# Kernel optimization log

Hardware: AMD Instinct MI355X
Metric: run time of the kernel (lower is better)

## Reference

```python
import jax, jax.numpy as jnp
import numpy as np

EPS = 1e-8
NEG = -1e9


def setup_inputs() -> dict:
    key = jax.random.key(0)
    k = jax.random.split(key, 5)
    B, C, T, D = 32, 512, 2000, 128
    return {
        "x": jax.random.normal(k[0], (B, C, T), dtype=jnp.float32),
        "attn_w": jax.random.normal(k[1], (D, 3 * C), dtype=jnp.float32) * 0.02,
        "attn_b": jax.random.normal(k[2], (D,), dtype=jnp.float32) * 0.02,
        "ctx_w": jax.random.normal(k[3], (C, D), dtype=jnp.float32) * 0.02,
        "ctx_b": jax.random.normal(k[4], (C,), dtype=jnp.float32) * 0.02,
        "mask": jnp.ones((B, T), dtype=jnp.int32),
    }


def reference(x, attn_w, attn_b, ctx_w, ctx_b, mask):
    # x: (B, C, T); mask: (B, T) with 1 = valid frame
    m = mask.astype(x.dtype)[:, None, :]                      # (B, 1, T)
    lengths = jnp.sum(m, axis=2, keepdims=True)               # (B, 1, 1)
    mean = jnp.sum(x * m, axis=2, keepdims=True) / lengths    # (B, C, 1)
    var = jnp.sum(jnp.square(x - mean) * m, axis=2, keepdims=True) / lengths
    std = jnp.sqrt(jnp.clip(var, EPS))                        # (B, C, 1)
    # global context: concat [x, mean, std] along channels -> (B, 3C, T)
    T = x.shape[2]
    context = jnp.concatenate(
        [x, jnp.broadcast_to(mean, x.shape), jnp.broadcast_to(std, x.shape)], axis=1
    )
    # two 1x1 convs == channel GEMMs
    alpha = jnp.tanh(jnp.einsum("dc,bct->bdt", attn_w, context) + attn_b[None, :, None])
    alpha = jnp.einsum("cd,bdt->bct", ctx_w, alpha) + ctx_b[None, :, None]  # (B, C, T)
    alpha = jnp.where(m == 0, NEG, alpha)
    alpha = jax.nn.softmax(alpha, axis=2)
    pooled_mean = jnp.sum(alpha * x, axis=2)                  # (B, C)
    pooled_var = jnp.sum(alpha * jnp.square(x - pooled_mean[:, :, None]), axis=2)
    pooled_std = jnp.sqrt(jnp.clip(pooled_var, EPS))
    return jnp.concatenate([pooled_mean, pooled_std], axis=1)  # (B, 2C)
```

## Files before the change

kernel.cpp:

```cpp
#include <hip/hip_runtime.h>
#include <hip/hip_bf16.h>
#include <math.h>

#define EPSF 1e-8f
typedef __attribute__((ext_vector_type(8))) short short8;
typedef __attribute__((ext_vector_type(4))) float f32x4;

__device__ __forceinline__ float wred_sum(float v) {
#pragma unroll
  for (int o = 32; o > 0; o >>= 1) v += __shfl_down(v, o, 64);
  return v;
}

static __device__ __forceinline__ unsigned short f2bf(float f) {
  __hip_bfloat16 h = __float2bfloat16(f);
  return *reinterpret_cast<unsigned short*>(&h);
}
static __device__ __forceinline__ float bf2f(unsigned short u) {
  unsigned int v = ((unsigned int)u) << 16;
  float f;
  __builtin_memcpy(&f, &v, 4);
  return f;
}

__global__ __launch_bounds__(256) void k_zc(
    const float* __restrict__ attn_w, const float* __restrict__ ctx_w,
    unsigned short* __restrict__ awb, unsigned short* __restrict__ cwb,
    float* __restrict__ zp, int nz4, int C, int D) {
  int i = blockIdx.x * 256 + threadIdx.x;
  int DC = D * C;
  if (i < DC) {
    int d = i / C, c = i % C;
    awb[i] = f2bf(attn_w[(size_t)d * 3 * C + c]);
  } else if (i < 2 * DC) {
    int j = i - DC;
    cwb[j] = f2bf(ctx_w[j]);
  }
  if (i < nz4)
    *reinterpret_cast<float4*>(zp + (size_t)i * 4) = (float4){0.f, 0.f, 0.f, 0.f};
}

__global__ __launch_bounds__(256) void k_ms_tr(
    const float* __restrict__ x, const int* __restrict__ mask,
    float* __restrict__ sums, unsigned short* __restrict__ xbT, int C, int T) {
  int b = blockIdx.z, c0 = blockIdx.x * 64, t0 = blockIdx.y * 64;
  int tid = threadIdx.x;
  int row = tid >> 2, q = tid & 3;
  __shared__ float Xs[64][65];
  const float* xr = x + ((size_t)b * C + c0 + row) * T;
  const int* mr = mask + (size_t)b * T;
  float s1 = 0.f, s2 = 0.f;

#pragma unroll
  for (int ss = 0; ss < 4; ss++) {
    int cc = q + 4 * ss;
    int t = t0 + cc * 4;
    float4 v;
    float mv[4];
    if (t + 3 < T) {
      v = *reinterpret_cast<const float4*>(&xr[t]);
      int4 mm = *reinterpret_cast<const int4*>(&mr[t]);
      mv[0] = (float)mm.x; mv[1] = (float)mm.y; mv[2] = (float)mm.z; mv[3] = (float)mm.w;
    } else {
      v.x = (t < T) ? xr[t] : 0.f;     mv[0] = (t < T) ? (float)mr[t] : 0.f;
      v.y = (t+1 < T) ? xr[t+1] : 0.f; mv[1] = (t+1 < T) ? (float)mr[t+1] : 0.f;
      v.z = (t+2 < T) ? xr[t+2] : 0.f; mv[2] = (t+2 < T) ? (float)mr[t+2] : 0.f;
      v.w = (t+3 < T) ? xr[t+3] : 0.f; mv[3] = (t+3 < T) ? (float)mr[t+3] : 0.f;
    }
    s1 += mv[0]*v.x + mv[1]*v.y + mv[2]*v.z + mv[3]*v.w;
    s2 += mv[0]*v.x*v.x + mv[1]*v.y*v.y + mv[2]*v.z*v.z + mv[3]*v.w*v.w;
    int tl = cc * 4;
    Xs[row][tl+0] = v.x; Xs[row][tl+1] = v.y; Xs[row][tl+2] = v.z; Xs[row][tl+3] = v.w;
  }
  __syncthreads();
  {
    int trow = tid >> 2;
    int t = t0 + trow;
    if (t < T) {
      unsigned short buf[16];
#pragma unroll
      for (int m = 0; m < 16; m++) buf[m] = f2bf(Xs[q * 16 + m][trow]);
      unsigned short* dst = &xbT[((size_t)b * T + t) * C + c0 + q * 16];
      *reinterpret_cast<short8*>(dst) = *reinterpret_cast<short8*>(&buf[0]);
      *reinterpret_cast<short8*>(dst + 8) = *reinterpret_cast<short8*>(&buf[8]);
    }
  }
  s1 += __shfl_down(s1, 2, 4); s1 += __shfl_down(s1, 1, 4);
  s2 += __shfl_down(s2, 2, 4); s2 += __shfl_down(s2, 1, 4);
  if (q == 0) {
    float* sp = &sums[((size_t)b * C + c0 + row) * 2];
    atomicAdd(sp, s1);
    atomicAdd(sp + 1, s2);
  }
}

__global__ __launch_bounds__(256) void k_bias2f(
    const float* __restrict__ attn_w, const float* __restrict__ attn_b,
    const float* __restrict__ sums, const int* __restrict__ mask,
    float* __restrict__ bias2, int C, int D, int T) {
  int bd = blockIdx.x;
  int b = bd / D;
  int d = bd % D;
  int tid = threadIdx.x;
  const int* mr = mask + (size_t)b * T;
  float sl = 0.f;
  for (int t = tid; t < T; t += 256) sl += (float)mr[t];
  __shared__ float rl[4];
  sl = wred_sum(sl);
  if ((tid & 63) == 0) rl[tid >> 6] = sl;
  __syncthreads();
  float L = fmaxf(rl[0] + rl[1] + rl[2] + rl[3], 1.f);

  const float* wr = attn_w + (size_t)d * 3 * C;
  float s = 0.f;
  for (int c = tid; c < C; c += 256) {
    float s1 = sums[((size_t)b * C + c) * 2];
    float s2 = sums[((size_t)b * C + c) * 2 + 1];
    float mu = s1 / L;
    float var = s2 / L - mu * mu;
    float sd = sqrtf(fmaxf(var, EPSF));
    s += wr[C + c] * mu + wr[2 * C + c] * sd;
  }
  __shared__ float r[4];
  s = wred_sum(s);
  if ((tid & 63) == 0) r[tid >> 6] = s;
  __syncthreads();
  if (tid == 0) bias2[bd] = attn_b[d] + r[0] + r[1] + r[2] + r[3];
}

__global__ __launch_bounds__(256) void k_gemm1(
    const unsigned short* __restrict__ xbT, const unsigned short* __restrict__ awb,
    const float* __restrict__ bias2, unsigned short* __restrict__ alphaT,
    int C, int T, int D) {
  int b = blockIdx.y;
  int t0 = blockIdx.x * 64;
  int tid = threadIdx.x;
  int w = tid >> 6, lane = tid & 63;
  int l15 = lane & 15, g = lane >> 4;
  __shared__ unsigned short As[64][72];
  __shared__ unsigned short Bs[128][72];
  f32x4 acc[4][2];
#pragma unroll
  for (int i = 0; i < 4; i++)
#pragma unroll
    for (int j = 0; j < 2; j++) acc[i][j] = (f32x4){0.f, 0.f, 0.f, 0.f};

  int ar = tid >> 2, aq = tid & 3;
  int dr = tid >> 1, h = tid & 1;
  bool okA = (t0 + ar) < T;
  size_t rowA = ((size_t)b * T + t0 + ar) * C + aq * 16;
  size_t rowB = (size_t)dr * C + h * 32;

  short8 ra[2], rb[4];
  ra[0] = okA ? *reinterpret_cast<const short8*>(&xbT[rowA]) : (short8){};
  ra[1] = okA ? *reinterpret_cast<const short8*>(&xbT[rowA + 8]) : (short8){};
#pragma unroll
  for (int qq = 0; qq < 4; qq++)
    rb[qq] = *reinterpret_cast<const short8*>(&awb[rowB + qq * 8]);

  for (int c0 = 0; c0 < C; c0 += 64) {
    __syncthreads();
    *reinterpret_cast<short8*>(&As[ar][aq * 16]) = ra[0];
    *reinterpret_cast<short8*>(&As[ar][aq * 16 + 8]) = ra[1];
#pragma unroll
    for (int qq = 0; qq < 4; qq++)
      *reinterpret_cast<short8*>(&Bs[dr][h * 32 + qq * 8]) = rb[qq];
    if (c0 + 64 < C) {
      size_t nA = rowA + c0 + 64, nB = rowB + c0 + 64;
      ra[0] = okA ? *reinterpret_cast<const short8*>(&xbT[nA]) : (short8){};
      ra[1] = okA ? *reinterpret_cast<const short8*>(&xbT[nA + 8]) : (short8){};
#pragma unroll
      for (int qq = 0; qq < 4; qq++)
        rb[qq] = *reinterpret_cast<const short8*>(&awb[nB + qq * 8]);
    }
    __syncthreads();
#pragma unroll
    for (int ks = 0; ks < 2; ks++) {
      short8 a[4], bb[2];
#pragma unroll
      for (int tf = 0; tf < 4; tf++)
        a[tf] = *reinterpret_cast<const short8*>(&As[tf * 16 + l15][ks * 32 + g * 8]);
#pragma unroll
      for (int df = 0; df < 2; df++)
        bb[df] = *reinterpret_cast<const short8*>(&Bs[w * 32 + df * 16 + l15][ks * 32 + g * 8]);
#pragma unroll
      for (int tf = 0; tf < 4; tf++)
#pragma unroll
        for (int df = 0; df < 2; df++)
          acc[tf][df] = __builtin_amdgcn_mfma_f32_16x16x32_bf16(a[tf], bb[df], acc[tf][df], 0, 0, 0);
    }
  }
#pragma unroll
  for (int df = 0; df < 2; df++) {
    int d = w * 32 + df * 16 + l15;
    float bias = bias2[(size_t)b * D + d];
#pragma unroll
    for (int tf = 0; tf < 4; tf++)
#pragma unroll
      for (int r = 0; r < 4; r++) {
        int t = t0 + tf * 16 + g * 4 + r;
        if (t < T)
          alphaT[((size_t)b * T + t) * D + d] = f2bf(tanhf(bias + acc[tf][df][r]));
      }
  }
}

__global__ __launch_bounds__(256) void k_pool2(
    const unsigned short* __restrict__ alphaT, const unsigned short* __restrict__ cwb,
    const unsigned short* __restrict__ xbT, const int* __restrict__ mask,
    float* __restrict__ Sacc, int C, int T, int D) {
  int b = blockIdx.z;
  int c0 = blockIdx.y * 64;
  int ch0 = blockIdx.x * 256;
  int tid = threadIdx.x;
  int w = tid >> 6, lane = tid & 63, l15 = lane & 15, g = lane >> 4;
  __shared__ unsigned short Bl[2][64][136];
  __shared__ unsigned short Xt[2][64][72];

  short8 a[4];
#pragma unroll
  for (int ks = 0; ks < 4; ks++)
    a[ks] = *reinterpret_cast<const short8*>(
        &cwb[(size_t)(c0 + w * 16 + l15) * D + ks * 32 + g * 8]);
  int cbase = c0 + w * 16 + g * 4;
  float S0[4] = {0.f, 0.f, 0.f, 0.f};
  float S1[4] = {0.f, 0.f, 0.f, 0.f};
  float S2[4] = {0.f, 0.f, 0.f, 0.f};

  const int* mr = mask + (size_t)b * T;
  int srow = tid >> 2, sq = tid & 3;

  int rem = T - ch0;
  int ntt = rem >= 256 ? 4 : (rem + 63) >> 6;

  short8 pa0, pa1, pa2, pa3, px0, px1;

#define LOADSUB(st)                                                            \
  {                                                                            \
    int trow = ch0 + (st) * 64 + srow;                                         \
    pa0 = pa1 = pa2 = pa3 = px0 = px1 = (short8){};                            \
    if (trow < T) {                                                            \
      const unsigned short* sa = &alphaT[((size_t)b * T + trow) * D + sq * 32];\
      pa0 = *reinterpret_cast<const short8*>(sa);                              \
      pa1 = *reinterpret_cast<const short8*>(sa + 8);                          \
      pa2 = *reinterpret_cast<const short8*>(sa + 16);                         \
      pa3 = *reinterpret_cast<const short8*>(sa + 24);                         \
      const unsigned short* sx = &xbT[((size_t)b * T + trow) * C + c0 + sq*16];\
      px0 = *reinterpret_cast<const short8*>(sx);                              \
      px1 = *reinterpret_cast<const short8*>(sx + 8);                          \
    }                                                                          \
  }

#define WRITESUB(bufi)                                                         \
  {                                                                            \
    *reinterpret_cast<short8*>(&Bl[bufi][srow][sq * 32]) = pa0;                \
    *reinterpret_cast<short8*>(&Bl[bufi][srow][sq * 32 + 8]) = pa1;            \
    *reinterpret_cast<short8*>(&Bl[bufi][srow][sq * 32 + 16]) = pa2;           \
    *reinterpret_cast<short8*>(&Bl[bufi][srow][sq * 32 + 24]) = pa3;           \
    *reinterpret_cast<short8*>(&Xt[bufi][srow][sq * 16]) = px0;                \
    *reinterpret_cast<short8*>(&Xt[bufi][srow][sq * 16 + 8]) = px1;            \
  }

  LOADSUB(0);
  WRITESUB(0);
  if (ntt > 1) LOADSUB(1);
  __syncthreads();

  for (int k = 0; k < ntt; k++) {
    int buf = k & 1;
    if (k + 1 < ntt) {
      WRITESUB((k + 1) & 1);
      if (k + 2 < ntt) LOADSUB(k + 2);
    }
    int t0 = ch0 + k * 64;
#pragma unroll
    for (int tf = 0; tf < 4; tf++) {
      f32x4 p = (f32x4){0.f, 0.f, 0.f, 0.f};
#pragma unroll
      for (int ks = 0; ks < 4; ks++) {
        short8 bb = *reinterpret_cast<const short8*>(
            &Bl[buf][tf * 16 + l15][ks * 32 + g * 8]);
        p = __builtin_amdgcn_mfma_f32_16x16x32_bf16(a[ks], bb, p, 0, 0, 0);
      }
      int t = t0 + tf * 16 + l15;
      bool valid = (t < T) && (mr[t < T ? t : 0] != 0);
#pragma unroll
      for (int r = 0; r < 4; r++) {
        float e = valid ? __expf(p[r]) : 0.f;
        float xv = bf2f(Xt[buf][tf * 16 + l15][w * 16 + g * 4 + r]);
        S0[r] += e; S1[r] += e * xv; S2[r] += e * xv * xv;
      }
    }
    __syncthreads();
  }
#undef LOADSUB
#undef WRITESUB

#pragma unroll
  for (int r = 0; r < 4; r++) {
#pragma unroll
    for (int o = 1; o < 16; o <<= 1) {
      S0[r] += __shfl_xor(S0[r], o, 16);
      S1[r] += __shfl_xor(S1[r], o, 16);
      S2[r] += __shfl_xor(S2[r], o, 16);
    }
  }
  if (l15 == 0) {
#pragma unroll
    for (int r = 0; r < 4; r++) {
      float* sp = &Sacc[((size_t)b * C + cbase + r) * 3];
      atomicAdd(sp, S0[r]);
      atomicAdd(sp + 1, S1[r]);
      atomicAdd(sp + 2, S2[r]);
    }
  }
}

__global__ __launch_bounds__(256) void k_out(
    const float* __restrict__ Sacc, float* __restrict__ out, int C) {
  int b = blockIdx.x;
  for (int c = threadIdx.x; c < C; c += 256) {
    float S0 = Sacc[((size_t)b * C + c) * 3];
    float S1 = Sacc[((size_t)b * C + c) * 3 + 1];
    float S2 = Sacc[((size_t)b * C + c) * 3 + 2];
    float pm = S1 / S0;
    float var = S2 / S0 - pm * pm;
    out[(size_t)b * 2 * C + c] = pm;
    out[(size_t)b * 2 * C + C + c] = sqrtf(fmaxf(var, EPSF));
  }
}

extern "C" void kernel_launch(void* const* d_in, const int* in_sizes, int n_in,
                              void* d_out, int out_size, void* d_ws, size_t ws_size,
                              hipStream_t stream) {
  const float* x = (const float*)d_in[0];
  const float* attn_w = (const float*)d_in[1];
  const float* attn_b = (const float*)d_in[2];
  const float* ctx_w = (const float*)d_in[3];
  const int* mask = (const int*)d_in[5];
  float* out = (float*)d_out;

  int D = in_sizes[2];
  int C = in_sizes[4];
  int B = out_size / (2 * C);
  int T = in_sizes[5] / B;

  unsigned short* awb = (unsigned short*)d_ws;
  unsigned short* cwb = awb + (size_t)D * C;
  float* bias2 = (float*)(cwb + (size_t)C * D);
  float* sums = bias2 + (size_t)B * D;
  float* Sacc = sums + (size_t)B * C * 2;
  unsigned short* xbT = (unsigned short*)(Sacc + (size_t)B * C * 3);
  unsigned short* alphaT = xbT + (size_t)B * T * C;

  int nz4 = (B * C * 5 + 3) / 4;
  int zcn = 2 * D * C > nz4 * 0 + 2 * D * C ? 2 * D * C : nz4;
  if (nz4 > zcn) zcn = nz4;
  k_zc<<<(zcn + 255) / 256, 256, 0, stream>>>(attn_w, ctx_w, awb, cwb, sums, nz4, C, D);
  k_ms_tr<<<dim3(C / 64, (T + 63) / 64, B), 256, 0, stream>>>(x, mask, sums, xbT, C, T);
  k_bias2f<<<B * D, 256, 0, stream>>>(attn_w, attn_b, sums, mask, bias2, C, D, T);
  k_gemm1<<<dim3((T + 63) / 64, B), 256, 0, stream>>>(xbT, awb, bias2, alphaT, C, T, D);
  k_pool2<<<dim3((T + 255) / 256, C / 64, B), 256, 0, stream>>>(
      alphaT, cwb, xbT, mask, Sacc, C, T, D);
  k_out<<<B, 256, 0, stream>>>(Sacc, out, C);
}
```

Before: 133.1 us.

## Widen pool kernel channel tile to 128 and read x directly from global

The pooling kernel now covers 128 channels per block, two 16-row MFMA fragments per wave, so each alpha tile staged in shared memory is reused for twice as many channels and the alphaT re-read across channel blocks is halved. The x values are no longer staged through shared memory; each lane loads its four-element slices straight from global memory per time row. This cuts LDS traffic and the number of blocks, but it raises register pressure, exposes global latency for the x loads inside the compute loop, and halves the grid size.

```diff
diff --git a/kernel.cpp b/kernel.cpp
--- a/kernel.cpp
+++ b/kernel.cpp
@@ -4,6 +4,7 @@
 
 #define EPSF 1e-8f
 typedef __attribute__((ext_vector_type(8))) short short8;
+typedef __attribute__((ext_vector_type(4))) short s4v;
 typedef __attribute__((ext_vector_type(4))) float f32x4;
 
 __device__ __forceinline__ float wred_sum(float v) {
@@ -210,22 +211,25 @@
     const unsigned short* __restrict__ xbT, const int* __restrict__ mask,
     float* __restrict__ Sacc, int C, int T, int D) {
   int b = blockIdx.z;
-  int c0 = blockIdx.y * 64;
+  int c0 = blockIdx.y * 128;
   int ch0 = blockIdx.x * 256;
   int tid = threadIdx.x;
   int w = tid >> 6, lane = tid & 63, l15 = lane & 15, g = lane >> 4;
   __shared__ unsigned short Bl[2][64][136];
-  __shared__ unsigned short Xt[2][64][72];
-
-  short8 a[4];
-#pragma unroll
-  for (int ks = 0; ks < 4; ks++)
-    a[ks] = *reinterpret_cast<const short8*>(
-        &cwb[(size_t)(c0 + w * 16 + l15) * D + ks * 32 + g * 8]);
-  int cbase = c0 + w * 16 + g * 4;
-  float S0[4] = {0.f, 0.f, 0.f, 0.f};
-  float S1[4] = {0.f, 0.f, 0.f, 0.f};
-  float S2[4] = {0.f, 0.f, 0.f, 0.f};
+
+  short8 a[2][4];
+#pragma unroll
+  for (int cf = 0; cf < 2; cf++)
+#pragma unroll
+    for (int ks = 0; ks < 4; ks++)
+      a[cf][ks] = *reinterpret_cast<const short8*>(
+          &cwb[(size_t)(c0 + w * 32 + cf * 16 + l15) * D + ks * 32 + g * 8]);
+  int cb0 = c0 + w * 32 + g * 4;
+  float S0[2][4], S1[2][4], S2[2][4];
+#pragma unroll
+  for (int cf = 0; cf < 2; cf++)
+#pragma unroll
+    for (int r = 0; r < 4; r++) { S0[cf][r] = 0.f; S1[cf][r] = 0.f; S2[cf][r] = 0.f; }
 
   const int* mr = mask + (size_t)b * T;
   int srow = tid >> 2, sq = tid & 3;
@@ -233,21 +237,18 @@
   int rem = T - ch0;
   int ntt = rem >= 256 ? 4 : (rem + 63) >> 6;
 
-  short8 pa0, pa1, pa2, pa3, px0, px1;
+  short8 pa0, pa1, pa2, pa3;
 
 #define LOADSUB(st)                                                            \
   {                                                                            \
     int trow = ch0 + (st) * 64 + srow;                                         \
-    pa0 = pa1 = pa2 = pa3 = px0 = px1 = (short8){};                            \
+    pa0 = pa1 = pa2 = pa3 = (short8){};                                        \
     if (trow < T) {                                                            \
       const unsigned short* sa = &alphaT[((size_t)b * T + trow) * D + sq * 32];\
       pa0 = *reinterpret_cast<const short8*>(sa);                              \
       pa1 = *reinterpret_cast<const short8*>(sa + 8);                          \
       pa2 = *reinterpret_cast<const short8*>(sa + 16);                         \
       pa3 = *reinterpret_cast<const short8*>(sa + 24);                         \
-      const unsigned short* sx = &xbT[((size_t)b * T + trow) * C + c0 + sq*16];\
-      px0 = *reinterpret_cast<const short8*>(sx);                              \
-      px1 = *reinterpret_cast<const short8*>(sx + 8);                          \
     }                                                                          \
   }
 
@@ -257,8 +258,6 @@
     *reinterpret_cast<short8*>(&Bl[bufi][srow][sq * 32 + 8]) = pa1;            \
     *reinterpret_cast<short8*>(&Bl[bufi][srow][sq * 32 + 16]) = pa2;           \
     *reinterpret_cast<short8*>(&Bl[bufi][srow][sq * 32 + 24]) = pa3;           \
-    *reinterpret_cast<short8*>(&Xt[bufi][srow][sq * 16]) = px0;                \
-    *reinterpret_cast<short8*>(&Xt[bufi][srow][sq * 16 + 8]) = px1;            \
   }
 
   LOADSUB(0);
@@ -275,20 +274,32 @@
     int t0 = ch0 + k * 64;
 #pragma unroll
     for (int tf = 0; tf < 4; tf++) {
-      f32x4 p = (f32x4){0.f, 0.f, 0.f, 0.f};
+      int t = t0 + tf * 16 + l15;
+      int tc = t < T ? t : T - 1;
+      bool valid = (t < T) && (mr[tc] != 0);
+      const unsigned short* xr = &xbT[((size_t)b * T + tc) * C];
+      s4v xv0 = *reinterpret_cast<const s4v*>(&xr[cb0]);
+      s4v xv1 = *reinterpret_cast<const s4v*>(&xr[cb0 + 16]);
+      short8 bb[4];
+#pragma unroll
+      for (int ks = 0; ks < 4; ks++)
+        bb[ks] = *reinterpret_cast<const short8*>(
+            &Bl[buf][tf * 16 + l15][ks * 32 + g * 8]);
+      f32x4 p0 = (f32x4){0.f, 0.f, 0.f, 0.f};
+      f32x4 p1 = (f32x4){0.f, 0.f, 0.f, 0.f};
 #pragma unroll
       for (int ks = 0; ks < 4; ks++) {
-        short8 bb = *reinterpret_cast<const short8*>(
-            &Bl[buf][tf * 16 + l15][ks * 32 + g * 8]);
-        p = __builtin_amdgcn_mfma_f32_16x16x32_bf16(a[ks], bb, p, 0, 0, 0);
-      }
-      int t = t0 + tf * 16 + l15;
-      bool valid = (t < T) && (mr[t < T ? t : 0] != 0);
+        p0 = __builtin_amdgcn_mfma_f32_16x16x32_bf16(a[0][ks], bb[ks], p0, 0, 0, 0);
+        p1 = __builtin_amdgcn_mfma_f32_16x16x32_bf16(a[1][ks], bb[ks], p1, 0, 0, 0);
+      }
 #pragma unroll
       for (int r = 0; r < 4; r++) {
-        float e = valid ? __expf(p[r]) : 0.f;
-        float xv = bf2f(Xt[buf][tf * 16 + l15][w * 16 + g * 4 + r]);
-        S0[r] += e; S1[r] += e * xv; S2[r] += e * xv * xv;
+        float e0 = valid ? __expf(p0[r]) : 0.f;
+        float e1 = valid ? __expf(p1[r]) : 0.f;
+        float x0 = bf2f((unsigned short)xv0[r]);
+        float x1 = bf2f((unsigned short)xv1[r]);
+        S0[0][r] += e0; S1[0][r] += e0 * x0; S2[0][r] += e0 * x0 * x0;
+        S0[1][r] += e1; S1[1][r] += e1 * x1; S2[1][r] += e1 * x1 * x1;
       }
     }
     __syncthreads();
@@ -297,22 +308,26 @@
 #undef WRITESUB
 
 #pragma unroll
-  for (int r = 0; r < 4; r++) {
-#pragma unroll
-    for (int o = 1; o < 16; o <<= 1) {
-      S0[r] += __shfl_xor(S0[r], o, 16);
-      S1[r] += __shfl_xor(S1[r], o, 16);
-      S2[r] += __shfl_xor(S2[r], o, 16);
-    }
-  }
+  for (int cf = 0; cf < 2; cf++)
+#pragma unroll
+    for (int r = 0; r < 4; r++) {
+#pragma unroll
+      for (int o = 1; o < 16; o <<= 1) {
+        S0[cf][r] += __shfl_xor(S0[cf][r], o, 16);
+        S1[cf][r] += __shfl_xor(S1[cf][r], o, 16);
+        S2[cf][r] += __shfl_xor(S2[cf][r], o, 16);
+      }
+    }
   if (l15 == 0) {
 #pragma unroll
-    for (int r = 0; r < 4; r++) {
-      float* sp = &Sacc[((size_t)b * C + cbase + r) * 3];
-      atomicAdd(sp, S0[r]);
-      atomicAdd(sp + 1, S1[r]);
-      atomicAdd(sp + 2, S2[r]);
-    }
+    for (int cf = 0; cf < 2; cf++)
+#pragma unroll
+      for (int r = 0; r < 4; r++) {
+        float* sp = &Sacc[((size_t)b * C + cb0 + cf * 16 + r) * 3];
+        atomicAdd(sp, S0[cf][r]);
+        atomicAdd(sp + 1, S1[cf][r]);
+        atomicAdd(sp + 2, S2[cf][r]);
+      }
   }
 }
 
@@ -354,13 +369,13 @@
   unsigned short* alphaT = xbT + (size_t)B * T * C;
 
   int nz4 = (B * C * 5 + 3) / 4;
-  int zcn = 2 * D * C > nz4 * 0 + 2 * D * C ? 2 * D * C : nz4;
+  int zcn = 2 * D * C;
   if (nz4 > zcn) zcn = nz4;
   k_zc<<<(zcn + 255) / 256, 256, 0, stream>>>(attn_w, ctx_w, awb, cwb, sums, nz4, C, D);
   k_ms_tr<<<dim3(C / 64, (T + 63) / 64, B), 256, 0, stream>>>(x, mask, sums, xbT, C, T);
   k_bias2f<<<B * D, 256, 0, stream>>>(attn_w, attn_b, sums, mask, bias2, C, D, T);
   k_gemm1<<<dim3((T + 63) / 64, B), 256, 0, stream>>>(xbT, awb, bias2, alphaT, C, T, D);
-  k_pool2<<<dim3((T + 255) / 256, C / 64, B), 256, 0, stream>>>(
+  k_pool2<<<dim3((T + 255) / 256, (C + 127) / 128, B), 256, 0, stream>>>(
       alphaT, cwb, xbT, mask, Sacc, C, T, D);
   k_out<<<B, 256, 0, stream>>>(Sacc, out, C);
 }
```

Result: slower. 136.4 us (+2.5%).

## Load x values directly into registers in pool kernel; precompute mask lengths once

Applied to the files above, without the earlier changes.

The pooling kernel stops staging x tiles through shared memory. Each lane now loads its own 4 bf16 channel values per time row straight from global memory into registers, double-buffered two sub-tiles ahead. Separately, the per-batch valid-length sum is computed once in the init kernel instead of in every one of the B*D bias blocks. The register path removes LDS writes and reads but issues narrow 8-byte global loads with a strided pattern, which may coalesce poorly.

```diff
diff --git a/kernel.cpp b/kernel.cpp
--- a/kernel.cpp
+++ b/kernel.cpp
@@ -4,6 +4,7 @@
 
 #define EPSF 1e-8f
 typedef __attribute__((ext_vector_type(8))) short short8;
+typedef __attribute__((ext_vector_type(4))) short s4v;
 typedef __attribute__((ext_vector_type(4))) float f32x4;
 
 __device__ __forceinline__ float wred_sum(float v) {
@@ -25,8 +26,9 @@
 
 __global__ __launch_bounds__(256) void k_zc(
     const float* __restrict__ attn_w, const float* __restrict__ ctx_w,
-    unsigned short* __restrict__ awb, unsigned short* __restrict__ cwb,
-    float* __restrict__ zp, int nz4, int C, int D) {
+    const int* __restrict__ mask, unsigned short* __restrict__ awb,
+    unsigned short* __restrict__ cwb, float* __restrict__ zp,
+    float* __restrict__ Lbuf, int nz4, int C, int D, int B, int T) {
   int i = blockIdx.x * 256 + threadIdx.x;
   int DC = D * C;
   if (i < DC) {
@@ -38,6 +40,17 @@
   }
   if (i < nz4)
     *reinterpret_cast<float4*>(zp + (size_t)i * 4) = (float4){0.f, 0.f, 0.f, 0.f};
+  if (blockIdx.x < B) {
+    int b = blockIdx.x;
+    const int* mr = mask + (size_t)b * T;
+    float sl = 0.f;
+    for (int t = threadIdx.x; t < T; t += 256) sl += (float)mr[t];
+    __shared__ float rl[4];
+    sl = wred_sum(sl);
+    if ((threadIdx.x & 63) == 0) rl[threadIdx.x >> 6] = sl;
+    __syncthreads();
+    if (threadIdx.x == 0) Lbuf[b] = rl[0] + rl[1] + rl[2] + rl[3];
+  }
 }
 
 __global__ __launch_bounds__(256) void k_ms_tr(
@@ -96,20 +109,13 @@
 
 __global__ __launch_bounds__(256) void k_bias2f(
     const float* __restrict__ attn_w, const float* __restrict__ attn_b,
-    const float* __restrict__ sums, const int* __restrict__ mask,
-    float* __restrict__ bias2, int C, int D, int T) {
+    const float* __restrict__ sums, const float* __restrict__ Lbuf,
+    float* __restrict__ bias2, int C, int D) {
   int bd = blockIdx.x;
   int b = bd / D;
   int d = bd % D;
   int tid = threadIdx.x;
-  const int* mr = mask + (size_t)b * T;
-  float sl = 0.f;
-  for (int t = tid; t < T; t += 256) sl += (float)mr[t];
-  __shared__ float rl[4];
-  sl = wred_sum(sl);
-  if ((tid & 63) == 0) rl[tid >> 6] = sl;
-  __syncthreads();
-  float L = fmaxf(rl[0] + rl[1] + rl[2] + rl[3], 1.f);
+  float L = fmaxf(Lbuf[b], 1.f);
 
   const float* wr = attn_w + (size_t)d * 3 * C;
   float s = 0.f;
@@ -215,7 +221,6 @@
   int tid = threadIdx.x;
   int w = tid >> 6, lane = tid & 63, l15 = lane & 15, g = lane >> 4;
   __shared__ unsigned short Bl[2][64][136];
-  __shared__ unsigned short Xt[2][64][72];
 
   short8 a[4];
 #pragma unroll
@@ -233,21 +238,20 @@
   int rem = T - ch0;
   int ntt = rem >= 256 ? 4 : (rem + 63) >> 6;
 
-  short8 pa0, pa1, pa2, pa3, px0, px1;
+  short8 pa0, pa1, pa2, pa3;
+  s4v xv[2][4];
+  const unsigned short* xbb = &xbT[(size_t)b * T * C];
 
 #define LOADSUB(st)                                                            \
   {                                                                            \
     int trow = ch0 + (st) * 64 + srow;                                         \
-    pa0 = pa1 = pa2 = pa3 = px0 = px1 = (short8){};                            \
+    pa0 = pa1 = pa2 = pa3 = (short8){};                                        \
     if (trow < T) {                                                            \
       const unsigned short* sa = &alphaT[((size_t)b * T + trow) * D + sq * 32];\
       pa0 = *reinterpret_cast<const short8*>(sa);                              \
       pa1 = *reinterpret_cast<const short8*>(sa + 8);                          \
       pa2 = *reinterpret_cast<const short8*>(sa + 16);                         \
       pa3 = *reinterpret_cast<const short8*>(sa + 24);                         \
-      const unsigned short* sx = &xbT[((size_t)b * T + trow) * C + c0 + sq*16];\
-      px0 = *reinterpret_cast<const short8*>(sx);                              \
-      px1 = *reinterpret_cast<const short8*>(sx + 8);                          \
     }                                                                          \
   }
 
@@ -257,16 +261,28 @@
     *reinterpret_cast<short8*>(&Bl[bufi][srow][sq * 32 + 8]) = pa1;            \
     *reinterpret_cast<short8*>(&Bl[bufi][srow][sq * 32 + 16]) = pa2;           \
     *reinterpret_cast<short8*>(&Bl[bufi][srow][sq * 32 + 24]) = pa3;           \
-    *reinterpret_cast<short8*>(&Xt[bufi][srow][sq * 16]) = px0;                \
-    *reinterpret_cast<short8*>(&Xt[bufi][srow][sq * 16 + 8]) = px1;            \
+  }
+
+#define GXV(pi, st)                                                            \
+  {                                                                            \
+    _Pragma("unroll")                                                          \
+    for (int tf_ = 0; tf_ < 4; tf_++) {                                        \
+      int t_ = ch0 + (st) * 64 + tf_ * 16 + l15;                               \
+      int tc_ = t_ < T ? t_ : T - 1;                                           \
+      xv[pi][tf_] = *reinterpret_cast<const s4v*>(&xbb[(size_t)tc_ * C + cbase]);\
+    }                                                                          \
   }
 
   LOADSUB(0);
   WRITESUB(0);
   if (ntt > 1) LOADSUB(1);
+  GXV(0, 0);
+  if (ntt > 1) GXV(1, 1);
   __syncthreads();
 
-  for (int k = 0; k < ntt; k++) {
+#pragma unroll
+  for (int k = 0; k < 4; k++) {
+    if (k >= ntt) break;
     int buf = k & 1;
     if (k + 1 < ntt) {
       WRITESUB((k + 1) & 1);
@@ -287,14 +303,16 @@
 #pragma unroll
       for (int r = 0; r < 4; r++) {
         float e = valid ? __expf(p[r]) : 0.f;
-        float xv = bf2f(Xt[buf][tf * 16 + l15][w * 16 + g * 4 + r]);
-        S0[r] += e; S1[r] += e * xv; S2[r] += e * xv * xv;
+        float xvf = bf2f((unsigned short)xv[buf][tf][r]);
+        S0[r] += e; S1[r] += e * xvf; S2[r] += e * xvf * xvf;
       }
     }
+    if (k + 2 < ntt) GXV(buf, k + 2);
     __syncthreads();
   }
 #undef LOADSUB
 #undef WRITESUB
+#undef GXV
 
 #pragma unroll
   for (int r = 0; r < 4; r++) {
@@ -348,17 +366,19 @@
   unsigned short* awb = (unsigned short*)d_ws;
   unsigned short* cwb = awb + (size_t)D * C;
   float* bias2 = (float*)(cwb + (size_t)C * D);
-  float* sums = bias2 + (size_t)B * D;
+  float* Lbuf = bias2 + (size_t)B * D;
+  float* sums = Lbuf + B;
   float* Sacc = sums + (size_t)B * C * 2;
   unsigned short* xbT = (unsigned short*)(Sacc + (size_t)B * C * 3);
   unsigned short* alphaT = xbT + (size_t)B * T * C;
 
   int nz4 = (B * C * 5 + 3) / 4;
-  int zcn = 2 * D * C > nz4 * 0 + 2 * D * C ? 2 * D * C : nz4;
+  int zcn = 2 * D * C;
   if (nz4 > zcn) zcn = nz4;
-  k_zc<<<(zcn + 255) / 256, 256, 0, stream>>>(attn_w, ctx_w, awb, cwb, sums, nz4, C, D);
+  k_zc<<<(zcn + 255) / 256, 256, 0, stream>>>(
+      attn_w, ctx_w, mask, awb, cwb, sums, Lbuf, nz4, C, D, B, T);
   k_ms_tr<<<dim3(C / 64, (T + 63) / 64, B), 256, 0, stream>>>(x, mask, sums, xbT, C, T);
-  k_bias2f<<<B * D, 256, 0, stream>>>(attn_w, attn_b, sums, mask, bias2, C, D, T);
+  k_bias2f<<<B * D, 256, 0, stream>>>(attn_w, attn_b, sums, Lbuf, bias2, C, D);
   k_gemm1<<<dim3((T + 63) / 64, B), 256, 0, stream>>>(xbT, awb, bias2, alphaT, C, T, D);
   k_pool2<<<dim3((T + 255) / 256, C / 64, B), 256, 0, stream>>>(
       alphaT, cwb, xbT, mask, Sacc, C, T, D);
```

Result: faster. 130.4 us (-2.1%).
